# Kernel optimization log

Measured on AMD Instinct MI355X. Metric: run time of the kernel, lower is better.

The kernel has to match this reference:

```python
import jax, jax.numpy as jnp
import numpy as np

M = 4096          # number of quadrature points
D_OBS = 64        # number of observation directions
KVALS = (0.5, 1.0, 1.5, 2.0)   # wavenumbers (init k_values)
N_ITER = 5        # Born iterations
C = 1.0 / (4.0 * np.pi)        # Green's function constant


def setup_inputs() -> dict:
    key = jax.random.key(0)
    k1, k2, k3, k4 = jax.random.split(key, 4)
    pts = jax.random.normal(k1, (M, 3), dtype=jnp.float32)
    weights = jax.random.uniform(k2, (M,), dtype=jnp.float32)
    V = jax.random.normal(k3, (M,), dtype=jnp.float32)
    obs_dirs = jax.random.normal(k4, (D_OBS, 3), dtype=jnp.float32)
    obs_dirs = obs_dirs / jnp.linalg.norm(obs_dirs, axis=1, keepdims=True)
    return {"V": V, "obs_dirs": obs_dirs, "pts": pts, "weights": weights}


def reference(V, obs_dirs, pts, weights):
    dtype = V.dtype
    dhat = jnp.array([0.0, 0.0, 1.0], dtype=dtype)  # default incident_dir, already unit
    dot_d = pts @ dhat                               # [M]
    r2 = jnp.sum(pts * pts, axis=1)                  # [M]

    # Pairwise distances; faithful to D2 = r2_i + r2_j - 2 pts_i . pts_j
    D2 = r2[:, None] + r2[None, :] - 2.0 * (pts @ pts.T)   # [M, M]
    D = jnp.sqrt(jnp.clip(D2, 1e-12, None))
    invD = 1.0 / jnp.clip(D, 1e-6, None)
    idx = jnp.arange(M)
    invD = jnp.where(idx[:, None] == idx[None, :], jnp.zeros((), dtype), invD)
    scale = C * invD                                  # [M, M]

    VW = V * weights                                  # [M]
    Q = pts @ obs_dirs.T                              # [M, D_OBS]

    outs = []
    for k in KVALS:
        # Green's-function kernel (same across Born iterations for fixed k)
        Gr = scale * jnp.cos(k * D)                   # [M, M]
        Gi = scale * jnp.sin(k * D)                   # [M, M]

        # incident plane wave psi0 = exp(i k r.dhat)
        p0r = jnp.cos(k * dot_d)
        p0i = jnp.sin(k * dot_d)
        pr, pi_ = p0r, p0i
        for _ in range(N_ITER):
            ar = pr * VW
            ai = pi_ * VW
            pr = p0r + (Gr @ ar - Gi @ ai)
            pi_ = p0i + (Gr @ ai + Gi @ ar)

        # far-field amplitude: f(k, obs) = -C * sum_j w_j V_j psi_j exp(-i k pts_j.obs)
        phr = jnp.cos(-k * Q)                         # [M, D_OBS]
        phi = jnp.sin(-k * Q)
        zr = V * pr                                   # [M]
        zi = V * pi_
        ir = zr[:, None] * phr - zi[:, None] * phi    # [M, D_OBS]
        ii = zr[:, None] * phi + zi[:, None] * phr
        fr = jnp.sum(ir * weights[:, None], axis=0)   # [D_OBS]
        fi = jnp.sum(ii * weights[:, None], axis=0)
        outs.append(jnp.stack([-C * fr, -C * fi], axis=-1))  # [D_OBS, 2]

    return jnp.stack(outs, axis=0)                    # [len(KVALS), D_OBS, 2]
```

## Files before the change

### kernel.cpp

```cpp
#include <hip/hip_runtime.h>


#define MM 4096
#define NK 4
#define CGREEN 0.07957747154594767f
#define INV2PI 0.15915494309189535f

#define OFF_VW   49152
#define OFF_P0R  53248
#define OFF_P0I  69632
#define OFF_YR   86016
#define OFF_YI   102400
#define OFF_PART 118784
#define NCHUNK 128
#define PART_FLOATS (NCHUNK * 8 * MM)
#define WS_NEED_PART ((size_t)(OFF_PART + PART_FLOATS) * 4)

typedef float f2 __attribute__((ext_vector_type(2)));

__device__ __forceinline__ f2 vfma(f2 a, f2 b, f2 c) {
    f2 r; r.x = fmaf(a.x, b.x, c.x); r.y = fmaf(a.y, b.y, c.y); return r;
}

__global__ __launch_bounds__(64) void init_k(const float* __restrict__ V,
                                             const float* __restrict__ pts,
                                             const float* __restrict__ w,
                                             float* __restrict__ ws) {
#pragma clang fp contract(off)
    int i = blockIdx.x * 64 + threadIdx.x;
    float x = pts[3 * i], y = pts[3 * i + 1], z = pts[3 * i + 2];
    float cvw = CGREEN * (V[i] * w[i]);
    float xx = x * x, yy = y * y, zz = z * z;
    float r2 = (xx + yy) + zz;
    float* cp = ws + i * 12;
    cp[0] = x; cp[1] = y; cp[2] = z; cp[3] = r2;
    ws[OFF_VW + i] = cvw;
#pragma unroll
    for (int n = 0; n < NK; n++) {
        float kk = 0.5f * (float)(n + 1);
        float s, c;
        sincosf(kk * z, &s, &c);
        ws[OFF_P0R + n * MM + i] = c;
        ws[OFF_P0I + n * MM + i] = s;
        cp[4 + n] = cvw * c;
        cp[8 + n] = cvw * s;
        ws[OFF_YR + n * MM + i] = 0.0f;
        ws[OFF_YI + n * MM + i] = 0.0f;
    }
}

__device__ __forceinline__ void body_col2(f2 rx, f2 ry, f2 rz, f2 rr2,
                                          int r0, int r1, int jg,
                                          float4 A, float4 R, float4 I,
                                          f2 acc0[4], f2 acc1[4]) {
    f2 d2;
    {
#pragma clang fp contract(off)
        f2 m; m.x = rx.x * A.x; m.y = rx.y * A.x;
        m = vfma(ry, (f2){A.y, A.y}, m);
        m = vfma(rz, (f2){A.z, A.z}, m);
        f2 r2s = rr2 + A.w;
        f2 twod = 2.0f * m;
        d2 = r2s - twod;
    }
    d2.x = fmaxf(d2.x, 1e-12f);
    d2.y = fmaxf(d2.y, 1e-12f);
    float ia = __builtin_amdgcn_rsqf(d2.x);
    float ib = __builtin_amdgcn_rsqf(d2.y);
    f2 invD = {ia, ib};
    f2 rev = d2 * invD * (0.5f * INV2PI);
    float sca = (jg == r0) ? 0.0f : ia;
    float scb = (jg == r1) ? 0.0f : ib;
    f2 s1, c1;
    s1.x = __builtin_amdgcn_sinf(rev.x);
    c1.x = __builtin_amdgcn_cosf(rev.x);
    s1.y = __builtin_amdgcn_sinf(rev.y);
    c1.y = __builtin_amdgcn_cosf(rev.y);
    f2 c2 = vfma(c1, c1, -(s1 * s1));
    f2 s2 = 2.0f * (c1 * s1);
    f2 c3 = vfma(c2, c1, -(s2 * s1));
    f2 s3 = vfma(s2, c1, c2 * s1);
    f2 c4 = vfma(c2, c2, -(s2 * s2));
    f2 s4 = 2.0f * (c2 * s2);
#define ACC_UPD(nn, CC, SS, ZR, ZI)                                          \
    {                                                                        \
        f2 ri = {ZR, ZI}, sw = {-ZI, ZR};                                    \
        f2 t0 = CC.x * ri; t0 = vfma((f2){SS.x, SS.x}, sw, t0);              \
        acc0[nn] = vfma((f2){sca, sca}, t0, acc0[nn]);                       \
        f2 t1 = CC.y * ri; t1 = vfma((f2){SS.y, SS.y}, sw, t1);              \
        acc1[nn] = vfma((f2){scb, scb}, t1, acc1[nn]);                       \
    }
    ACC_UPD(0, c1, s1, R.x, I.x)
    ACC_UPD(1, c2, s2, R.y, I.y)
    ACC_UPD(2, c3, s3, R.z, I.z)
    ACC_UPD(3, c4, s4, R.w, I.w)
#undef ACC_UPD
}

template <int C, bool USE_PART>
__global__ __launch_bounds__(256) void matvec_k(const float* __restrict__ cols,
                                                f2* __restrict__ part,
                                                float* __restrict__ yr,
                                                float* __restrict__ yi) {
    constexpr int TC = MM / C;
    const int chunk = blockIdx.x;
    const int rg = blockIdx.y;
    const int r0 = rg * 512 + threadIdx.x;
    const int r1 = r0 + 256;
    const float4 rowA = *(const float4*)&cols[r0 * 12];
    const float4 rowB = *(const float4*)&cols[r1 * 12];
    const f2 rx = {rowA.x, rowB.x}, ry = {rowA.y, rowB.y};
    const f2 rz = {rowA.z, rowB.z}, rr2 = {rowA.w, rowB.w};
    f2 acc0[4], acc1[4];
#pragma unroll
    for (int i = 0; i < 4; i++) {
        acc0[i].x = 0.0f; acc0[i].y = 0.0f;
        acc1[i].x = 0.0f; acc1[i].y = 0.0f;
    }
    const int jg0 = chunk * TC;
    const float* colbase = cols + (size_t)jg0 * 12;
#pragma unroll 4
    for (int j = 0; j < TC; j++) {
        const float4* cp = (const float4*)(colbase + j * 12);
        float4 A = cp[0], R = cp[1], I = cp[2];
        body_col2(rx, ry, rz, rr2, r0, r1, jg0 + j, A, R, I, acc0, acc1);
    }
    if (USE_PART) {
#pragma unroll
        for (int n = 0; n < NK; n++) {
            part[(size_t)(chunk * 4 + n) * MM + r0] = acc0[n];
            part[(size_t)(chunk * 4 + n) * MM + r1] = acc1[n];
        }
    } else {
#pragma unroll
        for (int n = 0; n < NK; n++) {
            atomicAdd(&yr[n * MM + r0], acc0[n].x);
            atomicAdd(&yi[n * MM + r0], acc0[n].y);
            atomicAdd(&yr[n * MM + r1], acc1[n].x);
            atomicAdd(&yi[n * MM + r1], acc1[n].y);
        }
    }
}

template <int C>
__global__ __launch_bounds__(256) void reduce_update_k(float* __restrict__ ws) {
    int t = blockIdx.x * 256 + threadIdx.x;
    int u = t & 7;
    int item = t >> 3;
    int row = item & (MM - 1);
    int n = item >> 12;
    const f2* part2 = (const f2*)(ws + OFF_PART);
    f2 s; s.x = 0.0f; s.y = 0.0f;
#pragma unroll
    for (int j = 0; j < C / 8; j++) {
        int c = u + 8 * j;
        s += part2[(size_t)(c * 4 + n) * MM + row];
    }
    s.x += __shfl_xor(s.x, 1); s.y += __shfl_xor(s.y, 1);
    s.x += __shfl_xor(s.x, 2); s.y += __shfl_xor(s.y, 2);
    s.x += __shfl_xor(s.x, 4); s.y += __shfl_xor(s.y, 4);
    if (u == 0) {
        float cvw = ws[OFF_VW + row];
        float pr = ws[OFF_P0R + n * MM + row] + s.x;
        float pi = ws[OFF_P0I + n * MM + row] + s.y;
        ws[row * 12 + 4 + n] = cvw * pr;
        ws[row * 12 + 8 + n] = cvw * pi;
    }
}

__global__ __launch_bounds__(256) void update_fallback_k(float* __restrict__ ws) {
    int i = blockIdx.x * 256 + threadIdx.x;
    float cvw = ws[OFF_VW + i];
#pragma unroll
    for (int n = 0; n < NK; n++) {
        float pr = ws[OFF_P0R + n * MM + i] + ws[OFF_YR + n * MM + i];
        float pi = ws[OFF_P0I + n * MM + i] + ws[OFF_YI + n * MM + i];
        ws[i * 12 + 4 + n] = cvw * pr;
        ws[i * 12 + 8 + n] = cvw * pi;
        ws[OFF_YR + n * MM + i] = 0.0f;
        ws[OFF_YI + n * MM + i] = 0.0f;
    }
}

__global__ __launch_bounds__(256) void far_k(const float* __restrict__ obs,
                                             const float* __restrict__ ws,
                                             float* __restrict__ out) {
    int kidx = (blockIdx.x >> 1) >> 6;
    int d = (blockIdx.x >> 1) & 63;
    int half = blockIdx.x & 1;
    float kk = 0.5f * (float)(kidx + 1);
    float ox = obs[3 * d], oy = obs[3 * d + 1], oz = obs[3 * d + 2];
    float fr = 0.0f, fi = 0.0f;
    for (int j = half * 2048 + threadIdx.x; j < half * 2048 + 2048; j += 256) {
        const float4* c4 = (const float4*)(ws + j * 12);
        float4 P = c4[0], AR = c4[1], AI = c4[2];
        float q = fmaf(P.z, oz, fmaf(P.y, oy, P.x * ox));
        float ar, ai;
        switch (kidx) {
            case 0: ar = AR.x; ai = AI.x; break;
            case 1: ar = AR.y; ai = AI.y; break;
            case 2: ar = AR.z; ai = AI.z; break;
            default: ar = AR.w; ai = AI.w; break;
        }
        float s, co;
        __sincosf(kk * q, &s, &co);
        fr += fmaf(ar, co,  ai * s);
        fi += fmaf(ai, co, -ar * s);
    }
#pragma unroll
    for (int off = 32; off > 0; off >>= 1) {
        fr += __shfl_down(fr, off);
        fi += __shfl_down(fi, off);
    }
    __shared__ float red[4][2];
    int wave = threadIdx.x >> 6;
    if ((threadIdx.x & 63) == 0) { red[wave][0] = fr; red[wave][1] = fi; }
    __syncthreads();
    if (threadIdx.x == 0) {
        fr = red[0][0] + red[1][0] + red[2][0] + red[3][0];
        fi = red[0][1] + red[1][1] + red[2][1] + red[3][1];
        atomicAdd(&out[(kidx * 64 + d) * 2 + 0], -fr);
        atomicAdd(&out[(kidx * 64 + d) * 2 + 1], -fi);
    }
}

extern "C" void kernel_launch(void* const* d_in, const int* in_sizes, int n_in,
                              void* d_out, int out_size, void* d_ws, size_t ws_size,
                              hipStream_t stream) {
    const float* V   = (const float*)d_in[0];
    const float* obs = (const float*)d_in[1];
    const float* pts = (const float*)d_in[2];
    const float* w   = (const float*)d_in[3];
    float* ws  = (float*)d_ws;
    float* out = (float*)d_out;

    hipMemsetAsync(out, 0, (size_t)out_size * 4, stream);

    init_k<<<64, 64, 0, stream>>>(V, pts, w, ws);
    if (ws_size >= WS_NEED_PART) {
        for (int it = 0; it < 5; it++) {
            matvec_k<NCHUNK, true><<<dim3(NCHUNK, 8), 256, 0, stream>>>(
                ws, (f2*)(ws + OFF_PART), ws + OFF_YR, ws + OFF_YI);
            reduce_update_k<NCHUNK><<<512, 256, 0, stream>>>(ws);
        }
    } else {
        for (int it = 0; it < 5; it++) {
            matvec_k<64, false><<<dim3(64, 8), 256, 0, stream>>>(
                ws, (f2*)(ws + OFF_PART), ws + OFF_YR, ws + OFF_YI);
            update_fallback_k<<<16, 256, 0, stream>>>(ws);
        }
    }
    far_k<<<512, 256, 0, stream>>>(obs, ws, out);
}
```

Baseline: 215.4 us.

## Fuse Born iterations into one persistent cooperative kernel with grid syncs

```diff
diff --git a/kernel.cpp b/kernel.cpp
--- a/kernel.cpp
+++ b/kernel.cpp
@@ -1,4 +1,5 @@
 #include <hip/hip_runtime.h>
+#include <hip/hip_cooperative_groups.h>
 
 
 #define MM 4096
@@ -13,37 +14,49 @@
 #define OFF_YI   102400
 #define OFF_PART 118784
 #define NCHUNK 128
+#define NBLK 512
 #define PART_FLOATS (NCHUNK * 8 * MM)
 #define WS_NEED_PART ((size_t)(OFF_PART + PART_FLOATS) * 4)
 
+namespace cg = cooperative_groups;
+
 typedef float f2 __attribute__((ext_vector_type(2)));
 
 __device__ __forceinline__ f2 vfma(f2 a, f2 b, f2 c) {
     f2 r; r.x = fmaf(a.x, b.x, c.x); r.y = fmaf(a.y, b.y, c.y); return r;
+}
+
+__device__ __forceinline__ void init_item(int i, int n, const float* __restrict__ V,
+                                          const float* __restrict__ pts,
+                                          const float* __restrict__ w,
+                                          float* __restrict__ ws, bool writeBase) {
+#pragma clang fp contract(off)
+    float x = pts[3 * i], y = pts[3 * i + 1], z = pts[3 * i + 2];
+    float cvw = CGREEN * (V[i] * w[i]);
+    float* cp = ws + i * 12;
+    if (writeBase) {
+        float xx = x * x, yy = y * y, zz = z * z;
+        float r2 = (xx + yy) + zz;
+        cp[0] = x; cp[1] = y; cp[2] = z; cp[3] = r2;
+        ws[OFF_VW + i] = cvw;
+    }
+    float kk = 0.5f * (float)(n + 1);
+    float s, c;
+    sincosf(kk * z, &s, &c);
+    ws[OFF_P0R + n * MM + i] = c;
+    ws[OFF_P0I + n * MM + i] = s;
+    cp[4 + n] = cvw * c;
+    cp[8 + n] = cvw * s;
 }
 
 __global__ __launch_bounds__(64) void init_k(const float* __restrict__ V,
                                              const float* __restrict__ pts,
                                              const float* __restrict__ w,
                                              float* __restrict__ ws) {
-#pragma clang fp contract(off)
     int i = blockIdx.x * 64 + threadIdx.x;
-    float x = pts[3 * i], y = pts[3 * i + 1], z = pts[3 * i + 2];
-    float cvw = CGREEN * (V[i] * w[i]);
-    float xx = x * x, yy = y * y, zz = z * z;
-    float r2 = (xx + yy) + zz;
-    float* cp = ws + i * 12;
-    cp[0] = x; cp[1] = y; cp[2] = z; cp[3] = r2;
-    ws[OFF_VW + i] = cvw;
 #pragma unroll
     for (int n = 0; n < NK; n++) {
-        float kk = 0.5f * (float)(n + 1);
-        float s, c;
-        sincosf(kk * z, &s, &c);
-        ws[OFF_P0R + n * MM + i] = c;
-        ws[OFF_P0I + n * MM + i] = s;
-        cp[4 + n] = cvw * c;
-        cp[8 + n] = cvw * s;
+        init_item(i, n, V, pts, w, ws, n == 0);
         ws[OFF_YR + n * MM + i] = 0.0f;
         ws[OFF_YI + n * MM + i] = 0.0f;
     }
@@ -224,6 +237,131 @@
     }
 }
 
+__global__ __launch_bounds__(256, 2) void born_k(const float* __restrict__ V,
+                                                 const float* __restrict__ pts,
+                                                 const float* __restrict__ w,
+                                                 const float* __restrict__ obs,
+                                                 float* __restrict__ ws,
+                                                 float* __restrict__ out,
+                                                 int out_n) {
+    constexpr int C = NCHUNK;
+    constexpr int TC = MM / C;
+    cg::grid_group grid = cg::this_grid();
+    const int bid = blockIdx.x;
+    const int tid = bid * 256 + threadIdx.x;
+
+    if (tid < MM * NK) {
+        int i = tid & (MM - 1);
+        int n = tid >> 12;
+        init_item(i, n, V, pts, w, ws, n == 0);
+    }
+    grid.sync();
+
+    const int cA = bid & 63;
+    const int rg = bid >> 6;
+    const int r0 = rg * 512 + threadIdx.x;
+    const int r1 = r0 + 256;
+    const float4 rowA = *(const float4*)&ws[r0 * 12];
+    const float4 rowB = *(const float4*)&ws[r1 * 12];
+    const f2 rx = {rowA.x, rowB.x}, ry = {rowA.y, rowB.y};
+    const f2 rz = {rowA.z, rowB.z}, rr2 = {rowA.w, rowB.w};
+
+    const int ru = tid & 7;
+    const int ritem = tid >> 3;
+    const int rrow = ritem & (MM - 1);
+    const int rn = ritem >> 12;
+    const float cvw_r = ws[OFF_VW + rrow];
+    const float p0r_r = ws[OFF_P0R + rn * MM + rrow];
+    const float p0i_r = ws[OFF_P0I + rn * MM + rrow];
+
+    f2* part = (f2*)(ws + OFF_PART);
+
+    for (int it = 0; it < 5; it++) {
+#pragma unroll
+        for (int h = 0; h < 2; h++) {
+            const int chunk = cA + 64 * h;
+            f2 acc0[4], acc1[4];
+#pragma unroll
+            for (int i = 0; i < 4; i++) {
+                acc0[i].x = 0.0f; acc0[i].y = 0.0f;
+                acc1[i].x = 0.0f; acc1[i].y = 0.0f;
+            }
+            const int jg0 = chunk * TC;
+            const float* colbase = ws + (size_t)jg0 * 12;
+#pragma unroll 4
+            for (int j = 0; j < TC; j++) {
+                const float4* cp = (const float4*)(colbase + j * 12);
+                float4 A = cp[0], R = cp[1], I = cp[2];
+                body_col2(rx, ry, rz, rr2, r0, r1, jg0 + j, A, R, I, acc0, acc1);
+            }
+#pragma unroll
+            for (int n = 0; n < NK; n++) {
+                part[(size_t)(chunk * 4 + n) * MM + r0] = acc0[n];
+                part[(size_t)(chunk * 4 + n) * MM + r1] = acc1[n];
+            }
+        }
+        grid.sync();
+
+        f2 s; s.x = 0.0f; s.y = 0.0f;
+#pragma unroll
+        for (int j = 0; j < C / 8; j++) {
+            int c = ru + 8 * j;
+            s += part[(size_t)(c * 4 + rn) * MM + rrow];
+        }
+        s.x += __shfl_xor(s.x, 1); s.y += __shfl_xor(s.y, 1);
+        s.x += __shfl_xor(s.x, 2); s.y += __shfl_xor(s.y, 2);
+        s.x += __shfl_xor(s.x, 4); s.y += __shfl_xor(s.y, 4);
+        if (ru == 0) {
+            float pr = p0r_r + s.x;
+            float pi = p0i_r + s.y;
+            ws[rrow * 12 + 4 + rn] = cvw_r * pr;
+            ws[rrow * 12 + 8 + rn] = cvw_r * pi;
+        }
+        if (it == 4 && tid < out_n) out[tid] = 0.0f;
+        grid.sync();
+    }
+
+    {
+        int kidx = (bid >> 1) >> 6;
+        int d = (bid >> 1) & 63;
+        int half = bid & 1;
+        float kk = 0.5f * (float)(kidx + 1);
+        float ox = obs[3 * d], oy = obs[3 * d + 1], oz = obs[3 * d + 2];
+        float fr = 0.0f, fi = 0.0f;
+        for (int j = half * 2048 + threadIdx.x; j < half * 2048 + 2048; j += 256) {
+            const float4* c4 = (const float4*)(ws + j * 12);
+            float4 P = c4[0], AR = c4[1], AI = c4[2];
+            float q = fmaf(P.z, oz, fmaf(P.y, oy, P.x * ox));
+            float ar, ai;
+            switch (kidx) {
+                case 0: ar = AR.x; ai = AI.x; break;
+                case 1: ar = AR.y; ai = AI.y; break;
+                case 2: ar = AR.z; ai = AI.z; break;
+                default: ar = AR.w; ai = AI.w; break;
+            }
+            float sn, co;
+            __sincosf(kk * q, &sn, &co);
+            fr += fmaf(ar, co,  ai * sn);
+            fi += fmaf(ai, co, -ar * sn);
+        }
+#pragma unroll
+        for (int off = 32; off > 0; off >>= 1) {
+            fr += __shfl_down(fr, off);
+            fi += __shfl_down(fi, off);
+        }
+        __shared__ float red[4][2];
+        int wave = threadIdx.x >> 6;
+        if ((threadIdx.x & 63) == 0) { red[wave][0] = fr; red[wave][1] = fi; }
+        __syncthreads();
+        if (threadIdx.x == 0) {
+            fr = red[0][0] + red[1][0] + red[2][0] + red[3][0];
+            fi = red[0][1] + red[1][1] + red[2][1] + red[3][1];
+            atomicAdd(&out[(kidx * 64 + d) * 2 + 0], -fr);
+            atomicAdd(&out[(kidx * 64 + d) * 2 + 1], -fi);
+        }
+    }
+}
+
 extern "C" void kernel_launch(void* const* d_in, const int* in_sizes, int n_in,
                               void* d_out, int out_size, void* d_ws, size_t ws_size,
                               hipStream_t stream) {
@@ -234,21 +372,39 @@
     float* ws  = (float*)d_ws;
     float* out = (float*)d_out;
 
-    hipMemsetAsync(out, 0, (size_t)out_size * 4, stream);
-
-    init_k<<<64, 64, 0, stream>>>(V, pts, w, ws);
     if (ws_size >= WS_NEED_PART) {
+        static int coop_ok = -1;
+        if (coop_ok < 0) {
+            int nb = 0;
+            hipError_t e = hipOccupancyMaxActiveBlocksPerMultiprocessor(
+                &nb, born_k, 256, 0);
+            coop_ok = (e == hipSuccess && nb >= 2) ? 1 : 0;
+        }
+        if (coop_ok == 1) {
+            int out_n = out_size;
+            void* args[] = {(void*)&V, (void*)&pts, (void*)&w, (void*)&obs,
+                            (void*)&ws, (void*)&out, (void*)&out_n};
+            hipError_t e = hipLaunchCooperativeKernel(
+                born_k, dim3(NBLK), dim3(256), args, 0, stream);
+            if (e == hipSuccess) return;
+            coop_ok = 0;
+        }
+        hipMemsetAsync(out, 0, (size_t)out_size * 4, stream);
+        init_k<<<64, 64, 0, stream>>>(V, pts, w, ws);
         for (int it = 0; it < 5; it++) {
             matvec_k<NCHUNK, true><<<dim3(NCHUNK, 8), 256, 0, stream>>>(
                 ws, (f2*)(ws + OFF_PART), ws + OFF_YR, ws + OFF_YI);
             reduce_update_k<NCHUNK><<<512, 256, 0, stream>>>(ws);
         }
+        far_k<<<512, 256, 0, stream>>>(obs, ws, out);
     } else {
+        hipMemsetAsync(out, 0, (size_t)out_size * 4, stream);
+        init_k<<<64, 64, 0, stream>>>(V, pts, w, ws);
         for (int it = 0; it < 5; it++) {
             matvec_k<64, false><<<dim3(64, 8), 256, 0, stream>>>(
                 ws, (f2*)(ws + OFF_PART), ws + OFF_YR, ws + OFF_YI);
             update_fallback_k<<<16, 256, 0, stream>>>(ws);
         }
-    }
-    far_k<<<512, 256, 0, stream>>>(obs, ws, out);
-}
+        far_k<<<512, 256, 0, stream>>>(obs, ws, out);
+    }
+}
```

Result: no change. 215.2 us (-0.1%).

## Cache base-wavenumber cos/sin Green matrix in workspace and reuse across Born iterations

Applied to the files above, without the earlier changes.

```diff
diff --git a/kernel.cpp b/kernel.cpp
--- a/kernel.cpp
+++ b/kernel.cpp
@@ -15,44 +15,60 @@
 #define NCHUNK 128
 #define PART_FLOATS (NCHUNK * 8 * MM)
 #define WS_NEED_PART ((size_t)(OFF_PART + PART_FLOATS) * 4)
+#define OFF_G    (OFF_PART + PART_FLOATS)
+#define G_FLOATS ((size_t)MM * MM * 2)
+#define WS_NEED_G (((size_t)OFF_G + G_FLOATS) * 4)
 
 typedef float f2 __attribute__((ext_vector_type(2)));
 
 __device__ __forceinline__ f2 vfma(f2 a, f2 b, f2 c) {
     f2 r; r.x = fmaf(a.x, b.x, c.x); r.y = fmaf(a.y, b.y, c.y); return r;
+}
+
+__device__ __forceinline__ void init_item(int i, int n, const float* __restrict__ V,
+                                          const float* __restrict__ pts,
+                                          const float* __restrict__ w,
+                                          float* __restrict__ ws, bool writeBase) {
+#pragma clang fp contract(off)
+    float x = pts[3 * i], y = pts[3 * i + 1], z = pts[3 * i + 2];
+    float cvw = CGREEN * (V[i] * w[i]);
+    float* cp = ws + i * 12;
+    if (writeBase) {
+        float xx = x * x, yy = y * y, zz = z * z;
+        float r2 = (xx + yy) + zz;
+        cp[0] = x; cp[1] = y; cp[2] = z; cp[3] = r2;
+        ws[OFF_VW + i] = cvw;
+    }
+    float kk = 0.5f * (float)(n + 1);
+    float s, c;
+    sincosf(kk * z, &s, &c);
+    ws[OFF_P0R + n * MM + i] = c;
+    ws[OFF_P0I + n * MM + i] = s;
+    cp[4 + n] = cvw * c;
+    cp[8 + n] = cvw * s;
 }
 
 __global__ __launch_bounds__(64) void init_k(const float* __restrict__ V,
                                              const float* __restrict__ pts,
                                              const float* __restrict__ w,
                                              float* __restrict__ ws) {
-#pragma clang fp contract(off)
     int i = blockIdx.x * 64 + threadIdx.x;
-    float x = pts[3 * i], y = pts[3 * i + 1], z = pts[3 * i + 2];
-    float cvw = CGREEN * (V[i] * w[i]);
-    float xx = x * x, yy = y * y, zz = z * z;
-    float r2 = (xx + yy) + zz;
-    float* cp = ws + i * 12;
-    cp[0] = x; cp[1] = y; cp[2] = z; cp[3] = r2;
-    ws[OFF_VW + i] = cvw;
 #pragma unroll
     for (int n = 0; n < NK; n++) {
-        float kk = 0.5f * (float)(n + 1);
-        float s, c;
-        sincosf(kk * z, &s, &c);
-        ws[OFF_P0R + n * MM + i] = c;
-        ws[OFF_P0I + n * MM + i] = s;
-        cp[4 + n] = cvw * c;
-        cp[8 + n] = cvw * s;
+        init_item(i, n, V, pts, w, ws, n == 0);
         ws[OFF_YR + n * MM + i] = 0.0f;
         ws[OFF_YI + n * MM + i] = 0.0f;
     }
 }
 
+template <int GM>
 __device__ __forceinline__ void body_col2(f2 rx, f2 ry, f2 rz, f2 rr2,
                                           int r0, int r1, int jg,
                                           float4 A, float4 R, float4 I,
-                                          f2 acc0[4], f2 acc1[4]) {
+                                          f2 acc0[4], f2 acc1[4],
+                                          float2* __restrict__ gcol) {
+    float2 ga, gb;
+    if (GM == 2) { ga = gcol[r0]; gb = gcol[r1]; }
     f2 d2;
     {
 #pragma clang fp contract(off)
@@ -67,15 +83,24 @@
     d2.y = fmaxf(d2.y, 1e-12f);
     float ia = __builtin_amdgcn_rsqf(d2.x);
     float ib = __builtin_amdgcn_rsqf(d2.y);
-    f2 invD = {ia, ib};
-    f2 rev = d2 * invD * (0.5f * INV2PI);
     float sca = (jg == r0) ? 0.0f : ia;
     float scb = (jg == r1) ? 0.0f : ib;
     f2 s1, c1;
-    s1.x = __builtin_amdgcn_sinf(rev.x);
-    c1.x = __builtin_amdgcn_cosf(rev.x);
-    s1.y = __builtin_amdgcn_sinf(rev.y);
-    c1.y = __builtin_amdgcn_cosf(rev.y);
+    if (GM == 2) {
+        c1.x = ga.x; s1.x = ga.y;
+        c1.y = gb.x; s1.y = gb.y;
+    } else {
+        f2 invD = {ia, ib};
+        f2 rev = d2 * invD * (0.5f * INV2PI);
+        s1.x = __builtin_amdgcn_sinf(rev.x);
+        c1.x = __builtin_amdgcn_cosf(rev.x);
+        s1.y = __builtin_amdgcn_sinf(rev.y);
+        c1.y = __builtin_amdgcn_cosf(rev.y);
+        if (GM == 1) {
+            gcol[r0] = make_float2(c1.x, s1.x);
+            gcol[r1] = make_float2(c1.y, s1.y);
+        }
+    }
     f2 c2 = vfma(c1, c1, -(s1 * s1));
     f2 s2 = 2.0f * (c1 * s1);
     f2 c3 = vfma(c2, c1, -(s2 * s1));
@@ -97,9 +122,10 @@
 #undef ACC_UPD
 }
 
-template <int C, bool USE_PART>
+template <int C, int GM, bool USE_PART>
 __global__ __launch_bounds__(256) void matvec_k(const float* __restrict__ cols,
                                                 f2* __restrict__ part,
+                                                float2* __restrict__ g2,
                                                 float* __restrict__ yr,
                                                 float* __restrict__ yi) {
     constexpr int TC = MM / C;
@@ -123,7 +149,8 @@
     for (int j = 0; j < TC; j++) {
         const float4* cp = (const float4*)(colbase + j * 12);
         float4 A = cp[0], R = cp[1], I = cp[2];
-        body_col2(rx, ry, rz, rr2, r0, r1, jg0 + j, A, R, I, acc0, acc1);
+        float2* gcol = g2 + (size_t)(jg0 + j) * MM;
+        body_col2<GM>(rx, ry, rz, rr2, r0, r1, jg0 + j, A, R, I, acc0, acc1, gcol);
     }
     if (USE_PART) {
 #pragma unroll
@@ -233,22 +260,35 @@
     const float* w   = (const float*)d_in[3];
     float* ws  = (float*)d_ws;
     float* out = (float*)d_out;
+    float2* g2 = (float2*)(ws + OFF_G);
+    f2* part = (f2*)(ws + OFF_PART);
 
     hipMemsetAsync(out, 0, (size_t)out_size * 4, stream);
 
     init_k<<<64, 64, 0, stream>>>(V, pts, w, ws);
-    if (ws_size >= WS_NEED_PART) {
+    if (ws_size >= WS_NEED_G) {
+        matvec_k<NCHUNK, 1, true><<<dim3(NCHUNK, 8), 256, 0, stream>>>(
+            ws, part, g2, ws + OFF_YR, ws + OFF_YI);
+        reduce_update_k<NCHUNK><<<512, 256, 0, stream>>>(ws);
+        for (int it = 1; it < 5; it++) {
+            matvec_k<NCHUNK, 2, true><<<dim3(NCHUNK, 8), 256, 0, stream>>>(
+                ws, part, g2, ws + OFF_YR, ws + OFF_YI);
+            reduce_update_k<NCHUNK><<<512, 256, 0, stream>>>(ws);
+        }
+        far_k<<<512, 256, 0, stream>>>(obs, ws, out);
+    } else if (ws_size >= WS_NEED_PART) {
         for (int it = 0; it < 5; it++) {
-            matvec_k<NCHUNK, true><<<dim3(NCHUNK, 8), 256, 0, stream>>>(
-                ws, (f2*)(ws + OFF_PART), ws + OFF_YR, ws + OFF_YI);
+            matvec_k<NCHUNK, 0, true><<<dim3(NCHUNK, 8), 256, 0, stream>>>(
+                ws, part, g2, ws + OFF_YR, ws + OFF_YI);
             reduce_update_k<NCHUNK><<<512, 256, 0, stream>>>(ws);
         }
+        far_k<<<512, 256, 0, stream>>>(obs, ws, out);
     } else {
         for (int it = 0; it < 5; it++) {
-            matvec_k<64, false><<<dim3(64, 8), 256, 0, stream>>>(
-                ws, (f2*)(ws + OFF_PART), ws + OFF_YR, ws + OFF_YI);
+            matvec_k<64, 0, false><<<dim3(64, 8), 256, 0, stream>>>(
+                ws, part, g2, ws + OFF_YR, ws + OFF_YI);
             update_fallback_k<<<16, 256, 0, stream>>>(ws);
         }
-    }
-    far_k<<<512, 256, 0, stream>>>(obs, ws, out);
-}
+        far_k<<<512, 256, 0, stream>>>(obs, ws, out);
+    }
+}
```

Measured after the change: 220.5 us. 2.4% more time.
